# Kernel optimization log

Hardware: AMD Instinct MI355X
Metric: run time of the kernel (lower is better)

## Reference

```python
import jax, jax.numpy as jnp
import numpy as np

N, D = 8192, 256
NUM_CLASSES = 64


def setup_inputs() -> dict:
    key = jax.random.key(0)
    k1, k2 = jax.random.split(key)
    represent = jax.random.normal(k1, (N, D), dtype=jnp.float32)
    label = jax.random.randint(k2, (N,), 0, NUM_CLASSES, dtype=jnp.int64)
    t = jnp.float32(0.1)  # temperature
    return {"represent": represent, "label": label, "t": t}


def reference(represent, label, t):
    x = represent.astype(jnp.float32)                      # [N, D]
    norms = jnp.sqrt(jnp.sum(x * x, axis=-1))              # [N]
    # pairwise cosine: (x x^T) / (||xi|| ||xj||)
    cos = (x @ x.T) / (norms[:, None] * norms[None, :])    # [N, N]
    pos_mask = label[:, None] == label[None, :]            # [N, N] bool
    e = jnp.exp(cos / t)                                   # [N, N]
    # original computes exp(mask * cos / t): masked-out entries become exp(0) = 1
    pos_pair = jnp.where(pos_mask, e, 1.0).sum(axis=-1)    # [N]
    neg_pair = jnp.where(pos_mask, 1.0, e).sum(axis=-1)    # [N]
    loss = (jnp.log(neg_pair) - jnp.log(pos_pair)).sum() / represent.shape[0]
    return loss
```

## Files before the change

### kernel.cpp

```cpp
#include <hip/hip_runtime.h>

#define N_ROWS 8192
#define DIM 256
#define NUM_CLASSES 64
#define NBLK 64
#define NTRI (NBLK * (NBLK + 1) / 2)
#define SCR_PITCH 36

typedef float f32x4 __attribute__((ext_vector_type(4)));

__device__ __forceinline__ void gload_lds16(const void* g, void* l) {
  __builtin_amdgcn_global_load_lds(
      (const __attribute__((address_space(1))) unsigned int*)g,
      (__attribute__((address_space(3))) unsigned int*)l, 16, 0, 0);
}

__device__ __forceinline__ void tri_decode(int q, int& I, int& J) {
  int i = (int)((129.0f - sqrtf(16641.0f - 8.0f * (float)q)) * 0.5f);
  while (i * (129 - i) / 2 > q) --i;
  while ((i + 1) * (128 - i) / 2 <= q) ++i;
  I = i;
  J = i + (q - i * (129 - i) / 2);
}

__global__ void __launch_bounds__(256) prep_kernel(
    const float* __restrict__ x, const float* __restrict__ tptr,
    unsigned int* __restrict__ xq, float* __restrict__ sv,
    float* __restrict__ gsum, unsigned int* __restrict__ gcnt) {
  if (blockIdx.x == 0 && threadIdx.x == 0) { *gsum = 0.f; *gcnt = 0u; }
  const int row = blockIdx.x * 4 + (threadIdx.x >> 6);
  const int lane = threadIdx.x & 63;
  const float4 v = *reinterpret_cast<const float4*>(x + (size_t)row * DIM + lane * 4);
  int p = __builtin_amdgcn_cvt_pk_fp8_f32(v.x, v.y, 0, false);
  p = __builtin_amdgcn_cvt_pk_fp8_f32(v.z, v.w, p, true);
  const float f0 = __builtin_amdgcn_cvt_f32_fp8(p, 0);
  const float f1 = __builtin_amdgcn_cvt_f32_fp8(p, 1);
  const float f2 = __builtin_amdgcn_cvt_f32_fp8(p, 2);
  const float f3 = __builtin_amdgcn_cvt_f32_fp8(p, 3);
  float ss = f0 * f0 + f1 * f1 + f2 * f2 + f3 * f3;
  xq[(size_t)row * 64 + lane] = (unsigned int)p;
  for (int m = 32; m; m >>= 1) ss += __shfl_xor(ss, m, 64);
  if (lane == 0) sv[row] = sqrtf(1.4426950408889634f / tptr[0] / ss);
}

__global__ void __launch_bounds__(256, 2) main_kernel(
    const unsigned char* __restrict__ xb, const float* __restrict__ sv,
    const int* __restrict__ lab, float2* __restrict__ part) {
  const int q = blockIdx.x;
  int I, J;
  tri_decode(q, I, J);
  const int rowBase = I * 128;
  const int colBase = J * 128;

  __shared__ alignas(16) unsigned char ldsbuf[65536];
  __shared__ float colred[2][128][2];
  __shared__ float rsv[128]; __shared__ int rlab[128];
  __shared__ float csv[128]; __shared__ int clab[128];
  unsigned char* Al = ldsbuf;
  unsigned char* Bl = ldsbuf + 32768;
  float* scr0 = reinterpret_cast<float*>(ldsbuf);
  float* scr1 = reinterpret_cast<float*>(ldsbuf + 18432);

  const int tid = threadIdx.x;
  const int wave = tid >> 6;
  const int lane = tid & 63;
  const int quad = lane >> 4;
  const int lc = lane & 15;
  const int wrow = (wave >> 1) * 64;
  const int wcol = (wave & 1) * 64;
  const int ch = wave & 1;
  const int lh = lane >> 4, l15 = lane & 15;

  if (tid < 128) {
    rsv[tid] = sv[rowBase + tid];
    rlab[tid] = lab[rowBase + tid];
    csv[tid] = sv[colBase + tid];
    clab[tid] = lab[colBase + tid];
  }

  const unsigned char* Ag = xb + (size_t)rowBase * DIM;
  const unsigned char* Bg = xb + (size_t)colBase * DIM;
#pragma unroll
  for (int i = 0; i < 8; ++i) {
    const int r = wave * 32 + i * 4 + lh;
    const int gseg = l15 ^ (r & 15);
    gload_lds16(Ag + (size_t)r * 256 + gseg * 16, Al + (wave * 32 + i * 4) * 256);
    gload_lds16(Bg + (size_t)r * 256 + gseg * 16, Bl + (wave * 32 + i * 4) * 256);
  }
  __syncthreads();

  f32x4 acc[4][4];
  const f32x4 zero4 = {0.f, 0.f, 0.f, 0.f};
  for (int mi = 0; mi < 4; ++mi)
    for (int ni = 0; ni < 4; ++ni) acc[mi][ni] = zero4;

  const int qh = quad >> 1, h8 = (quad & 1) * 8;
  int aOff[4], bOff[4];
#pragma unroll
  for (int mi = 0; mi < 4; ++mi)
    aOff[mi] = (wrow + mi * 16 + lc) * 256 + h8;
#pragma unroll
  for (int ni = 0; ni < 4; ++ni)
    bOff[ni] = (wcol + ni * 16 + lc) * 256 + h8;

#pragma unroll
  for (int kb = 0; kb < 8; ++kb) {
    const int swz = ((kb * 2 + qh) ^ lc) << 4;
    long afr[4], bfr[4];
#pragma unroll
    for (int mi = 0; mi < 4; ++mi)
      afr[mi] = *reinterpret_cast<const long*>(Al + aOff[mi] + swz);
#pragma unroll
    for (int ni = 0; ni < 4; ++ni)
      bfr[ni] = *reinterpret_cast<const long*>(Bl + bOff[ni] + swz);
#pragma unroll
    for (int mi = 0; mi < 4; ++mi)
#pragma unroll
      for (int ni = 0; ni < 4; ++ni)
        acc[mi][ni] = __builtin_amdgcn_mfma_f32_16x16x32_fp8_fp8(
            afr[mi], bfr[ni], acc[mi][ni], 0, 0, 0);
  }
  __syncthreads();

  float scol[4];
  int labc[4];
#pragma unroll
  for (int ni = 0; ni < 4; ++ni) {
    scol[ni] = csv[wcol + ni * 16 + lc];
    labc[ni] = clab[wcol + ni * 16 + lc];
  }
  float ctot[4] = {0.f, 0.f, 0.f, 0.f};
  float csame[4] = {0.f, 0.f, 0.f, 0.f};

#pragma unroll
  for (int mi = 0; mi < 4; ++mi) {
#pragma unroll
    for (int r = 0; r < 4; ++r) {
      const int lr = wrow + mi * 16 + quad * 4 + r;
      const float siv = rsv[lr];
      const int li = rlab[lr];
      float st = 0.f, sm = 0.f;
#pragma unroll
      for (int ni = 0; ni < 4; ++ni) {
        const float e = exp2f(acc[mi][ni][r] * (siv * scol[ni]));
        const float em = (li == labc[ni]) ? e : 0.f;
        st += e;
        sm += em;
        ctot[ni] += e;
        csame[ni] += em;
      }
      scr0[lr * SCR_PITCH + ch * 16 + lc] = st;
      scr1[lr * SCR_PITCH + ch * 16 + lc] = sm;
    }
  }

  if (J > I) {
#pragma unroll
    for (int ni = 0; ni < 4; ++ni) {
      float t2 = ctot[ni] + __shfl_xor(ctot[ni], 16, 64);
      t2 += __shfl_xor(t2, 32, 64);
      float s2 = csame[ni] + __shfl_xor(csame[ni], 16, 64);
      s2 += __shfl_xor(s2, 32, 64);
      if (quad == 0) {
        colred[0][wcol + ni * 16 + lc][wave >> 1] = t2;
        colred[1][wcol + ni * 16 + lc][wave >> 1] = s2;
      }
    }
  }
  __syncthreads();

  if (tid < 128) {
    const int base = tid * SCR_PITCH;
    f32x4 a0 = {0.f, 0.f, 0.f, 0.f}, a1 = {0.f, 0.f, 0.f, 0.f};
#pragma unroll
    for (int k = 0; k < 8; ++k)
      a0 += *reinterpret_cast<const f32x4*>(&scr0[base + 4 * k]);
#pragma unroll
    for (int k = 0; k < 8; ++k)
      a1 += *reinterpret_cast<const f32x4*>(&scr1[base + 4 * k]);
    float2 v;
    v.x = a0[0] + a0[1] + a0[2] + a0[3];
    v.y = a1[0] + a1[1] + a1[2] + a1[3];
    part[(size_t)J * N_ROWS + rowBase + tid] = v;
    if (J > I) {
      float2 w;
      w.x = colred[0][tid][0] + colred[0][tid][1];
      w.y = colred[1][tid][0] + colred[1][tid][1];
      part[(size_t)I * N_ROWS + colBase + tid] = w;
    }
  }
}

__global__ void __launch_bounds__(256) row_loss_kernel(
    const float2* __restrict__ part, const int* __restrict__ lab,
    float* __restrict__ gsum, unsigned int* __restrict__ gcnt,
    float* __restrict__ out) {
  __shared__ int h[NUM_CLASSES];
  if (threadIdx.x < NUM_CLASSES) h[threadIdx.x] = 0;
  __syncthreads();
  for (int i = threadIdx.x; i < N_ROWS; i += 256) atomicAdd(&h[lab[i]], 1);
  __syncthreads();

  const int row = blockIdx.x * 256 + threadIdx.x;
  float st = 0.f, sm = 0.f;
#pragma unroll 8
  for (int b = 0; b < 64; ++b) {
    const float2 v = part[(size_t)b * N_ROWS + row];
    st += v.x;
    sm += v.y;
  }
  const int c = h[lab[row]];
  const float pos = sm + (float)(N_ROWS - c);
  const float neg = (st - sm) + (float)c;
  float term = logf(neg) - logf(pos);
  for (int m = 32; m; m >>= 1) term += __shfl_xor(term, m, 64);
  __shared__ float wsum[4];
  const int lane = threadIdx.x & 63;
  const int wave = threadIdx.x >> 6;
  if (lane == 0) wsum[wave] = term;
  __syncthreads();
  if (threadIdx.x == 0) {
    atomicAdd(gsum, wsum[0] + wsum[1] + wsum[2] + wsum[3]);
    __threadfence();
    const unsigned int t = atomicAdd(gcnt, 1u);
    if (t == (unsigned int)(N_ROWS / 256 - 1)) {
      const float total = atomicAdd(gsum, 0.0f);
      out[0] = total * (1.0f / (float)N_ROWS);
    }
  }
}

extern "C" void kernel_launch(void* const* d_in, const int* in_sizes, int n_in,
                              void* d_out, int out_size, void* d_ws, size_t ws_size,
                              hipStream_t stream) {
  const float* x = (const float*)d_in[0];
  const int* lab = (const int*)d_in[1];
  const float* t = (const float*)d_in[2];
  float* out = (float*)d_out;

  char* ws = (char*)d_ws;
  unsigned int* xq = (unsigned int*)ws;
  float* sv = (float*)(ws + (2u << 20));
  float2* part = (float2*)(ws + (2u << 20) + (32u << 10));
  float* gsum = (float*)(ws + (6u << 20) + (32u << 10));
  unsigned int* gcnt = (unsigned int*)(ws + (6u << 20) + (32u << 10) + 8);

  prep_kernel<<<N_ROWS / 4, 256, 0, stream>>>(x, t, xq, sv, gsum, gcnt);
  main_kernel<<<NTRI, 256, 0, stream>>>((const unsigned char*)xq, sv, lab, part);
  row_loss_kernel<<<N_ROWS / 256, 256, 0, stream>>>(part, lab, gsum, gcnt, out);
}
```

Measured before the change: 106.2 us.

## Stage K dimension in two halves to shrink LDS and raise occupancy

The main GEMM tile now loads A and B in two K-halves of 128 bytes per row instead of the full 256, which roughly halves the LDS buffer. The swizzle changes from 16 to 8 segments to match. Launch bounds go from 2 to 3 blocks per CU so more blocks can be resident at once. In exchange, each block adds extra barriers and a serialized second load with no overlap against compute. The scratch reuse at offset 18432 still fits inside the 36864-byte buffer.

```diff
diff --git a/kernel.cpp b/kernel.cpp
--- a/kernel.cpp
+++ b/kernel.cpp
@@ -43,7 +43,7 @@
   if (lane == 0) sv[row] = sqrtf(1.4426950408889634f / tptr[0] / ss);
 }
 
-__global__ void __launch_bounds__(256, 2) main_kernel(
+__global__ void __launch_bounds__(256, 3) main_kernel(
     const unsigned char* __restrict__ xb, const float* __restrict__ sv,
     const int* __restrict__ lab, float2* __restrict__ part) {
   const int q = blockIdx.x;
@@ -52,14 +52,14 @@
   const int rowBase = I * 128;
   const int colBase = J * 128;
 
-  __shared__ alignas(16) unsigned char ldsbuf[65536];
+  __shared__ alignas(16) unsigned char buf[36864];
   __shared__ float colred[2][128][2];
   __shared__ float rsv[128]; __shared__ int rlab[128];
   __shared__ float csv[128]; __shared__ int clab[128];
-  unsigned char* Al = ldsbuf;
-  unsigned char* Bl = ldsbuf + 32768;
-  float* scr0 = reinterpret_cast<float*>(ldsbuf);
-  float* scr1 = reinterpret_cast<float*>(ldsbuf + 18432);
+  unsigned char* Al = buf;
+  unsigned char* Bl = buf + 16384;
+  float* scr0 = reinterpret_cast<float*>(buf);
+  float* scr1 = reinterpret_cast<float*>(buf + 18432);
 
   const int tid = threadIdx.x;
   const int wave = tid >> 6;
@@ -69,7 +69,8 @@
   const int wrow = (wave >> 1) * 64;
   const int wcol = (wave & 1) * 64;
   const int ch = wave & 1;
-  const int lh = lane >> 4, l15 = lane & 15;
+  const int r8 = lane >> 3;
+  const int c8 = lane & 7;
 
   if (tid < 128) {
     rsv[tid] = sv[rowBase + tid];
@@ -80,14 +81,18 @@
 
   const unsigned char* Ag = xb + (size_t)rowBase * DIM;
   const unsigned char* Bg = xb + (size_t)colBase * DIM;
-#pragma unroll
-  for (int i = 0; i < 8; ++i) {
-    const int r = wave * 32 + i * 4 + lh;
-    const int gseg = l15 ^ (r & 15);
-    gload_lds16(Ag + (size_t)r * 256 + gseg * 16, Al + (wave * 32 + i * 4) * 256);
-    gload_lds16(Bg + (size_t)r * 256 + gseg * 16, Bl + (wave * 32 + i * 4) * 256);
-  }
-  __syncthreads();
+
+#define STAGE_HALF(h)                                                         \
+  {                                                                           \
+    _Pragma("unroll") for (int i = 0; i < 4; ++i) {                           \
+      const int r = wave * 32 + i * 8 + r8;                                   \
+      const int gc = c8 ^ (r & 7);                                            \
+      gload_lds16(Ag + (size_t)r * 256 + (h)*128 + gc * 16,                   \
+                  Al + (wave * 32 + i * 8) * 128);                            \
+      gload_lds16(Bg + (size_t)r * 256 + (h)*128 + gc * 16,                   \
+                  Bl + (wave * 32 + i * 8) * 128);                            \
+    }                                                                         \
+  }
 
   f32x4 acc[4][4];
   const f32x4 zero4 = {0.f, 0.f, 0.f, 0.f};
@@ -98,29 +103,39 @@
   int aOff[4], bOff[4];
 #pragma unroll
   for (int mi = 0; mi < 4; ++mi)
-    aOff[mi] = (wrow + mi * 16 + lc) * 256 + h8;
+    aOff[mi] = (wrow + mi * 16 + lc) * 128 + h8;
 #pragma unroll
   for (int ni = 0; ni < 4; ++ni)
-    bOff[ni] = (wcol + ni * 16 + lc) * 256 + h8;
-
-#pragma unroll
-  for (int kb = 0; kb < 8; ++kb) {
-    const int swz = ((kb * 2 + qh) ^ lc) << 4;
-    long afr[4], bfr[4];
-#pragma unroll
-    for (int mi = 0; mi < 4; ++mi)
-      afr[mi] = *reinterpret_cast<const long*>(Al + aOff[mi] + swz);
-#pragma unroll
-    for (int ni = 0; ni < 4; ++ni)
-      bfr[ni] = *reinterpret_cast<const long*>(Bl + bOff[ni] + swz);
-#pragma unroll
-    for (int mi = 0; mi < 4; ++mi)
+    bOff[ni] = (wcol + ni * 16 + lc) * 128 + h8;
+
+  STAGE_HALF(0)
+  __syncthreads();
+#pragma unroll
+  for (int half = 0; half < 2; ++half) {
+#pragma unroll
+    for (int kbl = 0; kbl < 4; ++kbl) {
+      const int swz = (((kbl * 2 + qh) ^ (lc & 7)) << 4);
+      long afr[4], bfr[4];
+#pragma unroll
+      for (int mi = 0; mi < 4; ++mi)
+        afr[mi] = *reinterpret_cast<const long*>(Al + aOff[mi] + swz);
 #pragma unroll
       for (int ni = 0; ni < 4; ++ni)
-        acc[mi][ni] = __builtin_amdgcn_mfma_f32_16x16x32_fp8_fp8(
-            afr[mi], bfr[ni], acc[mi][ni], 0, 0, 0);
-  }
-  __syncthreads();
+        bfr[ni] = *reinterpret_cast<const long*>(Bl + bOff[ni] + swz);
+#pragma unroll
+      for (int mi = 0; mi < 4; ++mi)
+#pragma unroll
+        for (int ni = 0; ni < 4; ++ni)
+          acc[mi][ni] = __builtin_amdgcn_mfma_f32_16x16x32_fp8_fp8(
+              afr[mi], bfr[ni], acc[mi][ni], 0, 0, 0);
+    }
+    __syncthreads();
+    if (half == 0) {
+      STAGE_HALF(1)
+      __syncthreads();
+    }
+  }
+#undef STAGE_HALF
 
   float scol[4];
   int labc[4];
```

Result: faster. 98.62 us (-7.1%).
